# Optimization experiments

Hardware: AMD Instinct MI355X
Metric: run time of the kernel (lower is better)

## Reference

```python
import jax, jax.numpy as jnp
import numpy as np

EPS = 1e-5

def _ln(x, g, b):
    mu = jnp.mean(x, axis=-1, keepdims=True)
    var = jnp.mean(jnp.square(x - mu), axis=-1, keepdims=True)
    return (x - mu) * jax.lax.rsqrt(var + EPS) * g + b

def _gelu_new(x):
    # GPT-2 'gelu_new' (tanh approximation)
    c = jnp.asarray(np.sqrt(2.0 / np.pi), x.dtype)
    return 0.5 * x * (1.0 + jnp.tanh(c * (x + 0.044715 * x * x * x)))

def setup_inputs() -> dict:
    key = jax.random.key(0)
    ks = jax.random.split(key, 8)
    B, H, NH, HD, S = 16, 2048, 16, 128, 4096
    inv = lambda n: 1.0 / np.sqrt(n)
    return {
        "hidden_states": jax.random.normal(ks[0], (B, 1, H), jnp.float32),
        "cached_k": jax.random.normal(ks[1], (B, NH, S, HD), jnp.float32),
        "cached_v": jax.random.normal(ks[2], (B, NH, S, HD), jnp.float32),
        "ln1_g": jnp.ones((H,), jnp.float32),
        "ln1_b": jnp.zeros((H,), jnp.float32),
        "W_qkv": jax.random.normal(ks[3], (H, 3 * H), jnp.float32) * inv(H),
        "b_qkv": jnp.zeros((3 * H,), jnp.float32),
        "W_proj": jax.random.normal(ks[4], (H, H), jnp.float32) * inv(H),
        "b_proj": jnp.zeros((H,), jnp.float32),
        "ln2_g": jnp.ones((H,), jnp.float32),
        "ln2_b": jnp.zeros((H,), jnp.float32),
        "W_fc": jax.random.normal(ks[5], (H, 4 * H), jnp.float32) * inv(H),
        "b_fc": jnp.zeros((4 * H,), jnp.float32),
        "W_out": jax.random.normal(ks[6], (4 * H, H), jnp.float32) * inv(4 * H),
        "b_out": jnp.zeros((H,), jnp.float32),
    }

def reference(hidden_states, cached_k, cached_v, ln1_g, ln1_b, W_qkv, b_qkv,
              W_proj, b_proj, ln2_g, ln2_b, W_fc, b_fc, W_out, b_out):
    B, T, H = hidden_states.shape  # T == 1 (decode step)
    NH, HD = cached_k.shape[1], cached_k.shape[3]
    residual = hidden_states
    x = _ln(hidden_states, ln1_g, ln1_b)
    qkv = x @ W_qkv + b_qkv                        # [B,1,3H]
    q, k, v = jnp.split(qkv, 3, axis=-1)
    split = lambda t: t.reshape(B, T, NH, HD).transpose(0, 2, 1, 3)  # [B,NH,T,HD]
    q, k, v = split(q), split(k), split(v)
    k_full = jnp.concatenate([cached_k, k], axis=2)  # [B,NH,S+1,HD]
    v_full = jnp.concatenate([cached_v, v], axis=2)
    scale = 1.0 / jnp.sqrt(jnp.asarray(HD, q.dtype))
    scores = jnp.einsum('bhqd,bhkd->bhqk', q, k_full) * scale
    probs = jax.nn.softmax(scores, axis=-1)
    attn = jnp.einsum('bhqk,bhkd->bhqd', probs, v_full)  # [B,NH,1,HD]
    attn = attn.transpose(0, 2, 1, 3).reshape(B, T, H)
    attn = attn @ W_proj + b_proj
    h = attn + residual
    residual = h
    y = _ln(h, ln2_g, ln2_b)
    y = _gelu_new(y @ W_fc + b_fc) @ W_out + b_out
    return residual + y
```

## Files before the change

kernel.cpp:

```cpp
#include <hip/hip_runtime.h>
#include <hip/hip_bf16.h>

typedef unsigned int uint;


__global__ __launch_bounds__(256) void ln_f32_kernel(const float* __restrict__ in,
    const float* __restrict__ g, const float* __restrict__ bb, float* __restrict__ out)
{
    int row = blockIdx.x, t = threadIdx.x;
    const float* rp = in + row*2048;
    float4 a = ((const float4*)rp)[2*t];
    float4 b = ((const float4*)rp)[2*t+1];
    float v[8] = {a.x,a.y,a.z,a.w,b.x,b.y,b.z,b.w};
    float s=0.f, s2=0.f;
    #pragma unroll
    for(int i=0;i<8;i++){ s+=v[i]; s2+=v[i]*v[i]; }
    #pragma unroll
    for(int o=32;o>0;o>>=1){ s += __shfl_xor(s,o); s2 += __shfl_xor(s2,o); }
    __shared__ float red[8];
    int wv=t>>6, ln=t&63;
    if(ln==0){ red[wv]=s; red[4+wv]=s2; }
    __syncthreads();
    s  = red[0]+red[1]+red[2]+red[3];
    s2 = red[4]+red[5]+red[6]+red[7];
    float mu = s*(1.f/2048.f);
    float var = s2*(1.f/2048.f) - mu*mu;
    float rs = rsqrtf(var + 1e-5f);
    float4 g0 = ((const float4*)g)[2*t],  g1 = ((const float4*)g)[2*t+1];
    float4 b0 = ((const float4*)bb)[2*t], b1 = ((const float4*)bb)[2*t+1];
    float* op = out + row*2048 + t*8;
    float4 o0 = make_float4((v[0]-mu)*rs*g0.x+b0.x, (v[1]-mu)*rs*g0.y+b0.y,
                            (v[2]-mu)*rs*g0.z+b0.z, (v[3]-mu)*rs*g0.w+b0.w);
    float4 o1 = make_float4((v[4]-mu)*rs*g1.x+b1.x, (v[5]-mu)*rs*g1.y+b1.y,
                            (v[6]-mu)*rs*g1.z+b1.z, (v[7]-mu)*rs*g1.w+b1.w);
    ((float4*)op)[0]=o0; ((float4*)op)[1]=o1;
}

template<int KCHUNK>
__global__ __launch_bounds__(256) void gemm_sk(const float* __restrict__ X,
    const float* __restrict__ W, float* __restrict__ part, int K, int N, int colchunks)
{
    __shared__ float XS[16][KCHUNK];
    int cc = blockIdx.x % colchunks;
    int kc = blockIdx.x / colchunks;
    int k0 = kc * KCHUNK;
    for (int idx = threadIdx.x; idx < 16*KCHUNK; idx += 256){
        int m = idx / KCHUNK, i = idx % KCHUNK;
        XS[m][i] = X[m*K + k0 + i];
    }
    __syncthreads();
    int n0 = cc*512 + threadIdx.x*2;
    float a0[16], a1[16];
    #pragma unroll
    for(int m=0;m<16;m++){ a0[m]=0.f; a1[m]=0.f; }
    const float* Wp = W + (size_t)k0*N + n0;
    for (int i=0;i<KCHUNK;i+=4){
        float2 w0 = *(const float2*)(Wp + (size_t)(i+0)*N);
        float2 w1 = *(const float2*)(Wp + (size_t)(i+1)*N);
        float2 w2 = *(const float2*)(Wp + (size_t)(i+2)*N);
        float2 w3 = *(const float2*)(Wp + (size_t)(i+3)*N);
        #pragma unroll
        for(int m=0;m<16;m++){
            float4 x4 = *(const float4*)&XS[m][i];
            a0[m] += x4.x*w0.x + x4.y*w1.x + x4.z*w2.x + x4.w*w3.x;
            a1[m] += x4.x*w0.y + x4.y*w1.y + x4.z*w2.y + x4.w*w3.y;
        }
    }
    #pragma unroll
    for(int m=0;m<16;m++){
        *(float2*)&part[((size_t)(kc*16+m))*N + n0] = make_float2(a0[m], a1[m]);
    }
}

__global__ __launch_bounds__(256) void reduce_sk(const float* __restrict__ part, int N, int splitk,
    const float* __restrict__ bias, const float* __restrict__ res,
    float* __restrict__ outf, int mode)
{
    int n = blockIdx.x*256 + threadIdx.x;
    int m = blockIdx.y;
    size_t stride = (size_t)16*N;
    const float* p = part + (size_t)m*N + n;
    float s = 0.f;
    for (int kc=0;kc<splitk;kc++) s += p[(size_t)kc*stride];
    s += bias[n];
    if (mode==1 || mode==3) s += res[m*N+n];
    if (mode==2){
        float x = s;
        float t = tanhf(0.7978845608028654f*(x + 0.044715f*x*x*x));
        s = 0.5f*x*(1.f+t);
    }
    outf[m*N+n] = s;
}

__global__ __launch_bounds__(256) void attn_chunk(const float* __restrict__ qkv,
    const float* __restrict__ Kc, const float* __restrict__ Vc, float* __restrict__ part)
{
    int h = blockIdx.y, b = blockIdx.z;
    int wave = threadIdx.x >> 6, lane = threadIdx.x & 63;
    int wc = blockIdx.x*4 + wave;
    int grp = lane >> 4, cl = lane & 15;
    const float* qrow = qkv + b*6144 + h*128 + cl*8;
    float4 qa = *(const float4*)qrow;
    float4 qb = *(const float4*)(qrow + 4);
    size_t bh = (size_t)(b*16+h);
    size_t base = bh*524288 + (size_t)wc*16384 + (size_t)grp*128 + cl*8;
    const float* Kp = Kc + base;
    const float* Vp = Vc + base;

    float s[32];
    #pragma unroll
    for (int i=0;i<32;i++){
        const float* kp = Kp + (size_t)i*512;
        float4 ka = *(const float4*)kp;
        float4 kb = *(const float4*)(kp + 4);
        float p = qa.x*ka.x + qa.y*ka.y + qa.z*ka.z + qa.w*ka.w
                + qb.x*kb.x + qb.y*kb.y + qb.z*kb.z + qb.w*kb.w;
        p += __shfl_xor(p,1); p += __shfl_xor(p,2);
        p += __shfl_xor(p,4); p += __shfl_xor(p,8);
        s[i] = p * 0.08838834764831845f;
    }
    float m = s[0];
    #pragma unroll
    for (int i=1;i<32;i++) m = fmaxf(m, s[i]);
    m = fmaxf(m, __shfl_xor(m,16));
    m = fmaxf(m, __shfl_xor(m,32));

    float sn = 0.f;
    if (wc == 31){
        const float* kn = qkv + b*6144 + 2048 + h*128 + cl*8;
        float4 ka = *(const float4*)kn, kb = *(const float4*)(kn+4);
        float p = qa.x*ka.x + qa.y*ka.y + qa.z*ka.z + qa.w*ka.w
                + qb.x*kb.x + qb.y*kb.y + qb.z*kb.z + qb.w*kb.w;
        p += __shfl_xor(p,1); p += __shfl_xor(p,2);
        p += __shfl_xor(p,4); p += __shfl_xor(p,8);
        sn = p * 0.08838834764831845f;
        m = fmaxf(m, sn);
    }

    float l = 0.f;
    #pragma unroll
    for (int i=0;i<32;i++){ s[i] = __expf(s[i] - m); l += s[i]; }

    float o[8];
    #pragma unroll
    for (int i=0;i<8;i++) o[i] = 0.f;
    #pragma unroll
    for (int i=0;i<32;i++){
        const float* vp = Vp + (size_t)i*512;
        float4 va = *(const float4*)vp;
        float4 vb = *(const float4*)(vp + 4);
        float e = s[i];
        o[0]+=e*va.x; o[1]+=e*va.y; o[2]+=e*va.z; o[3]+=e*va.w;
        o[4]+=e*vb.x; o[5]+=e*vb.y; o[6]+=e*vb.z; o[7]+=e*vb.w;
    }
    if (wc == 31){
        const float* vn = qkv + b*6144 + 4096 + h*128 + cl*8;
        float4 va = *(const float4*)vn, vb = *(const float4*)(vn+4);
        float e = (grp==0) ? __expf(sn - m) : 0.f;
        l += e;
        o[0]+=e*va.x; o[1]+=e*va.y; o[2]+=e*va.z; o[3]+=e*va.w;
        o[4]+=e*vb.x; o[5]+=e*vb.y; o[6]+=e*vb.z; o[7]+=e*vb.w;
    }

    l += __shfl_xor(l,16); l += __shfl_xor(l,32);
    #pragma unroll
    for(int i=0;i<8;i++){ o[i] += __shfl_xor(o[i],16); o[i] += __shfl_xor(o[i],32); }
    float* pp = part + ((size_t)bh*32 + wc)*136;
    if (lane==0){ pp[0]=m; pp[1]=l; }
    if (lane<16){
        *(float4*)&pp[4 + lane*8]     = make_float4(o[0],o[1],o[2],o[3]);
        *(float4*)&pp[4 + lane*8 + 4] = make_float4(o[4],o[5],o[6],o[7]);
    }
}

__global__ __launch_bounds__(64) void attn_combine(const float* __restrict__ part,
                                                   float* __restrict__ attn_out)
{
    int bh = blockIdx.x;
    int lane = threadIdx.x;
    const float* pp = part + (size_t)bh*32*136;
    float M = -1e30f;
    for (int kc=0;kc<32;kc++) M = fmaxf(M, pp[kc*136]);
    float den=0.f, a0=0.f, a1=0.f;
    for (int kc=0;kc<32;kc++){
        float f = __expf(pp[kc*136] - M);
        den += f * pp[kc*136+1];
        float2 o = *(const float2*)&pp[kc*136 + 4 + 2*lane];
        a0 += f*o.x; a1 += f*o.y;
    }
    float inv = 1.f/den;
    int b = bh>>4, h = bh&15;
    float* op = attn_out + b*2048 + h*128 + 2*lane;
    op[0]=a0*inv; op[1]=a1*inv;
}

extern "C" void kernel_launch(void* const* d_in, const int* in_sizes, int n_in,
                              void* d_out, int out_size, void* d_ws, size_t ws_size,
                              hipStream_t stream)
{
    const float* hid  = (const float*)d_in[0];
    const float* Kc   = (const float*)d_in[1];
    const float* Vc   = (const float*)d_in[2];
    const float* ln1g = (const float*)d_in[3];
    const float* ln1b = (const float*)d_in[4];
    const float* Wqkv = (const float*)d_in[5];
    const float* bqkv = (const float*)d_in[6];
    const float* Wproj= (const float*)d_in[7];
    const float* bproj= (const float*)d_in[8];
    const float* ln2g = (const float*)d_in[9];
    const float* ln2b = (const float*)d_in[10];
    const float* Wfc  = (const float*)d_in[11];
    const float* bfc  = (const float*)d_in[12];
    const float* Wout = (const float*)d_in[13];
    const float* bout = (const float*)d_in[14];

    float* ws      = (float*)d_ws;
    float* xln     = ws;
    float* qkv     = xln + 32768;
    float* attn_o  = qkv + 98304;
    float* hbuf    = attn_o + 32768;
    float* yln     = hbuf + 32768;
    float* act     = yln + 32768;
    float* apart   = act + 131072;
    float* gpart   = apart + 1114112;

    ln_f32_kernel<<<16,256,0,stream>>>(hid, ln1g, ln1b, xln);
    gemm_sk<64><<<12*32,256,0,stream>>>(xln, Wqkv, gpart, 2048, 6144, 12);
    reduce_sk<<<dim3(24,16),256,0,stream>>>(gpart, 6144, 32, bqkv, nullptr, qkv, 0);
    attn_chunk<<<dim3(8,16,16),256,0,stream>>>(qkv, Kc, Vc, apart);
    attn_combine<<<256,64,0,stream>>>(apart, attn_o);
    gemm_sk<64><<<4*32,256,0,stream>>>(attn_o, Wproj, gpart, 2048, 2048, 4);
    reduce_sk<<<dim3(8,16),256,0,stream>>>(gpart, 2048, 32, bproj, hid, hbuf, 1);
    ln_f32_kernel<<<16,256,0,stream>>>(hbuf, ln2g, ln2b, yln);
    gemm_sk<64><<<16*32,256,0,stream>>>(yln, Wfc, gpart, 2048, 8192, 16);
    reduce_sk<<<dim3(32,16),256,0,stream>>>(gpart, 8192, 32, bfc, nullptr, act, 2);
    gemm_sk<128><<<4*64,256,0,stream>>>(act, Wout, gpart, 8192, 2048, 4);
    reduce_sk<<<dim3(8,16),256,0,stream>>>(gpart, 2048, 64, bout, hbuf, (float*)d_out, 3);
    (void)in_sizes; (void)n_in; (void)out_size; (void)ws_size;
}
```

Measured before the change: 399.4 us.

## Fuse attention chunk and combine into one block per head

Replaces the split-KV attention (2048 blocks writing partials, then a separate combine kernel) with one 1024-thread block per (batch, head). Each wave strides over keys and owns 64 of them. The waves combine max, sum and output through shared memory, which removes the partial-buffer round trip and one launch. The trade-off is only 256 blocks for a memory-bound scan of 1 GB of KV, which lowers parallelism. Each thread also now keeps 64 scores in registers, which may raise register pressure.

```diff
diff --git a/kernel.cpp b/kernel.cpp
--- a/kernel.cpp
+++ b/kernel.cpp
@@ -92,25 +92,24 @@
     outf[m*N+n] = s;
 }
 
-__global__ __launch_bounds__(256) void attn_chunk(const float* __restrict__ qkv,
-    const float* __restrict__ Kc, const float* __restrict__ Vc, float* __restrict__ part)
-{
-    int h = blockIdx.y, b = blockIdx.z;
-    int wave = threadIdx.x >> 6, lane = threadIdx.x & 63;
-    int wc = blockIdx.x*4 + wave;
+__global__ __launch_bounds__(1024) void attn_fused(const float* __restrict__ qkv,
+    const float* __restrict__ Kc, const float* __restrict__ Vc, float* __restrict__ attn_o)
+{
+    int bh = blockIdx.x;
+    int b = bh >> 4, h = bh & 15;
+    int w = threadIdx.x >> 6, lane = threadIdx.x & 63;
     int grp = lane >> 4, cl = lane & 15;
     const float* qrow = qkv + b*6144 + h*128 + cl*8;
     float4 qa = *(const float4*)qrow;
     float4 qb = *(const float4*)(qrow + 4);
-    size_t bh = (size_t)(b*16+h);
-    size_t base = bh*524288 + (size_t)wc*16384 + (size_t)grp*128 + cl*8;
+    size_t base = (size_t)bh*524288 + (size_t)(w*4 + grp)*128 + cl*8;
     const float* Kp = Kc + base;
     const float* Vp = Vc + base;
 
-    float s[32];
-    #pragma unroll
-    for (int i=0;i<32;i++){
-        const float* kp = Kp + (size_t)i*512;
+    float s[64];
+    #pragma unroll
+    for (int i=0;i<64;i++){
+        const float* kp = Kp + (size_t)i*8192;
         float4 ka = *(const float4*)kp;
         float4 kb = *(const float4*)(kp + 4);
         float p = qa.x*ka.x + qa.y*ka.y + qa.z*ka.z + qa.w*ka.w
@@ -119,14 +118,8 @@
         p += __shfl_xor(p,4); p += __shfl_xor(p,8);
         s[i] = p * 0.08838834764831845f;
     }
-    float m = s[0];
-    #pragma unroll
-    for (int i=1;i<32;i++) m = fmaxf(m, s[i]);
-    m = fmaxf(m, __shfl_xor(m,16));
-    m = fmaxf(m, __shfl_xor(m,32));
-
-    float sn = 0.f;
-    if (wc == 31){
+    float sn = -1e30f;
+    if (w == 0){
         const float* kn = qkv + b*6144 + 2048 + h*128 + cl*8;
         float4 ka = *(const float4*)kn, kb = *(const float4*)(kn+4);
         float p = qa.x*ka.x + qa.y*ka.y + qa.z*ka.z + qa.w*ka.w
@@ -134,64 +127,63 @@
         p += __shfl_xor(p,1); p += __shfl_xor(p,2);
         p += __shfl_xor(p,4); p += __shfl_xor(p,8);
         sn = p * 0.08838834764831845f;
-        m = fmaxf(m, sn);
-    }
+    }
+    float mw = s[0];
+    #pragma unroll
+    for (int i=1;i<64;i++) mw = fmaxf(mw, s[i]);
+    mw = fmaxf(mw, __shfl_xor(mw,16));
+    mw = fmaxf(mw, __shfl_xor(mw,32));
+    if (w == 0) mw = fmaxf(mw, sn);
+    __shared__ float lm[16], ll[16], lo[16][128];
+    if (lane == 0) lm[w] = mw;
+    __syncthreads();
+    float M = lm[0];
+    #pragma unroll
+    for (int i=1;i<16;i++) M = fmaxf(M, lm[i]);
 
     float l = 0.f;
     #pragma unroll
-    for (int i=0;i<32;i++){ s[i] = __expf(s[i] - m); l += s[i]; }
+    for (int i=0;i<64;i++){ s[i] = __expf(s[i] - M); l += s[i]; }
 
     float o[8];
     #pragma unroll
     for (int i=0;i<8;i++) o[i] = 0.f;
     #pragma unroll
-    for (int i=0;i<32;i++){
-        const float* vp = Vp + (size_t)i*512;
+    for (int i=0;i<64;i++){
+        const float* vp = Vp + (size_t)i*8192;
         float4 va = *(const float4*)vp;
         float4 vb = *(const float4*)(vp + 4);
         float e = s[i];
         o[0]+=e*va.x; o[1]+=e*va.y; o[2]+=e*va.z; o[3]+=e*va.w;
         o[4]+=e*vb.x; o[5]+=e*vb.y; o[6]+=e*vb.z; o[7]+=e*vb.w;
     }
-    if (wc == 31){
+    if (w == 0 && grp == 0){
         const float* vn = qkv + b*6144 + 4096 + h*128 + cl*8;
         float4 va = *(const float4*)vn, vb = *(const float4*)(vn+4);
-        float e = (grp==0) ? __expf(sn - m) : 0.f;
+        float e = __expf(sn - M);
         l += e;
         o[0]+=e*va.x; o[1]+=e*va.y; o[2]+=e*va.z; o[3]+=e*va.w;
         o[4]+=e*vb.x; o[5]+=e*vb.y; o[6]+=e*vb.z; o[7]+=e*vb.w;
     }
-
     l += __shfl_xor(l,16); l += __shfl_xor(l,32);
     #pragma unroll
-    for(int i=0;i<8;i++){ o[i] += __shfl_xor(o[i],16); o[i] += __shfl_xor(o[i],32); }
-    float* pp = part + ((size_t)bh*32 + wc)*136;
-    if (lane==0){ pp[0]=m; pp[1]=l; }
-    if (lane<16){
-        *(float4*)&pp[4 + lane*8]     = make_float4(o[0],o[1],o[2],o[3]);
-        *(float4*)&pp[4 + lane*8 + 4] = make_float4(o[4],o[5],o[6],o[7]);
-    }
-}
-
-__global__ __launch_bounds__(64) void attn_combine(const float* __restrict__ part,
-                                                   float* __restrict__ attn_out)
-{
-    int bh = blockIdx.x;
-    int lane = threadIdx.x;
-    const float* pp = part + (size_t)bh*32*136;
-    float M = -1e30f;
-    for (int kc=0;kc<32;kc++) M = fmaxf(M, pp[kc*136]);
-    float den=0.f, a0=0.f, a1=0.f;
-    for (int kc=0;kc<32;kc++){
-        float f = __expf(pp[kc*136] - M);
-        den += f * pp[kc*136+1];
-        float2 o = *(const float2*)&pp[kc*136 + 4 + 2*lane];
-        a0 += f*o.x; a1 += f*o.y;
-    }
-    float inv = 1.f/den;
-    int b = bh>>4, h = bh&15;
-    float* op = attn_out + b*2048 + h*128 + 2*lane;
-    op[0]=a0*inv; op[1]=a1*inv;
+    for (int i=0;i<8;i++){ o[i] += __shfl_xor(o[i],16); o[i] += __shfl_xor(o[i],32); }
+    if (lane == 0) ll[w] = l;
+    if (lane < 16){
+        #pragma unroll
+        for (int k=0;k<8;k++) lo[w][cl*8 + k] = o[k];
+    }
+    __syncthreads();
+    if (threadIdx.x < 128){
+        int d = threadIdx.x;
+        float L = 0.f;
+        #pragma unroll
+        for (int i=0;i<16;i++) L += ll[i];
+        float od = 0.f;
+        #pragma unroll
+        for (int i=0;i<16;i++) od += lo[i][d];
+        attn_o[b*2048 + h*128 + d] = od / L;
+    }
 }
 
 extern "C" void kernel_launch(void* const* d_in, const int* in_sizes, int n_in,
@@ -221,14 +213,12 @@
     float* hbuf    = attn_o + 32768;
     float* yln     = hbuf + 32768;
     float* act     = yln + 32768;
-    float* apart   = act + 131072;
-    float* gpart   = apart + 1114112;
+    float* gpart   = act + 131072;
 
     ln_f32_kernel<<<16,256,0,stream>>>(hid, ln1g, ln1b, xln);
     gemm_sk<64><<<12*32,256,0,stream>>>(xln, Wqkv, gpart, 2048, 6144, 12);
     reduce_sk<<<dim3(24,16),256,0,stream>>>(gpart, 6144, 32, bqkv, nullptr, qkv, 0);
-    attn_chunk<<<dim3(8,16,16),256,0,stream>>>(qkv, Kc, Vc, apart);
-    attn_combine<<<256,64,0,stream>>>(apart, attn_o);
+    attn_fused<<<256,1024,0,stream>>>(qkv, Kc, Vc, attn_o);
     gemm_sk<64><<<4*32,256,0,stream>>>(attn_o, Wproj, gpart, 2048, 2048, 4);
     reduce_sk<<<dim3(8,16),256,0,stream>>>(gpart, 2048, 32, bproj, hid, hbuf, 1);
     ln_f32_kernel<<<16,256,0,stream>>>(hbuf, ln2g, ln2b, yln);
```

Measured after the change: 417.2 us. 1.04x slower.
